# Kernel optimization log

Hardware: AMD Instinct MI355X
Metric: run time of the kernel (lower is better)

The kernel has to match this reference:

```python
import jax, jax.numpy as jnp
import numpy as np

V, S, D, H, L = 32000, 2048, 768, 12, 6
HD = D // H
EPS = 1e-5


def _sinusoidal_pe(s, d):
    pos = np.arange(s)[:, None].astype(np.float32)
    div = np.exp(np.arange(0, d, 2).astype(np.float32) * (-np.log(10000.0) / d))
    pe = np.zeros((s, d), dtype=np.float32)
    pe[:, 0::2] = np.sin(pos * div)
    pe[:, 1::2] = np.cos(pos * div)
    return jnp.asarray(pe)


def setup_inputs() -> dict:
    key = jax.random.key(0)
    ks = jax.random.split(key, 16)
    std = 0.02
    tok_emb = jax.random.normal(ks[0], (V, D), jnp.float32) * std
    tok_emb = tok_emb.at[1].set(0.0)  # padding_idx=1
    pos_enc = _sinusoidal_pe(S, D)
    attn_w = jax.random.normal(ks[1], (L, 3 * D, D), jnp.float32) * std
    attn_b = jnp.zeros((L, 3 * D), jnp.float32)
    proj_std = 0.02 / np.sqrt(2 * 6)
    proj_w = jax.random.normal(ks[2], (L, D, D), jnp.float32) * proj_std
    proj_b = jnp.zeros((L, D), jnp.float32)
    ln1_g = jnp.ones((L, D), jnp.float32); ln1_b = jnp.zeros((L, D), jnp.float32)
    ln2_g = jnp.ones((L, D), jnp.float32); ln2_b = jnp.zeros((L, D), jnp.float32)
    fc1_w = jax.random.normal(ks[3], (L, 4 * D, D), jnp.float32) * std
    fc1_b = jnp.zeros((L, 4 * D), jnp.float32)
    fc2_w = jax.random.normal(ks[4], (L, D, 4 * D), jnp.float32) * std
    fc2_b = jnp.zeros((L, D), jnp.float32)
    dec_w = jax.random.normal(ks[5], (V, D), jnp.float32) * std
    idx = jax.random.randint(ks[6], (2, S), 0, V)
    return dict(idx=idx, tok_emb=tok_emb, pos_enc=pos_enc, attn_w=attn_w,
                attn_b=attn_b, proj_w=proj_w, proj_b=proj_b, ln1_g=ln1_g,
                ln1_b=ln1_b, ln2_g=ln2_g, ln2_b=ln2_b, fc1_w=fc1_w,
                fc1_b=fc1_b, fc2_w=fc2_w, fc2_b=fc2_b, dec_w=dec_w)


def _ln(x, g, b):
    mu = jnp.mean(x, -1, keepdims=True)
    var = jnp.mean(jnp.square(x - mu), -1, keepdims=True)
    return (x - mu) * jax.lax.rsqrt(var + EPS) * g + b


def _forward(idx, tok_emb, pos_enc, attn_w, attn_b, proj_w, proj_b,
             ln1_g, ln1_b, ln2_g, ln2_b, fc1_w, fc1_b, fc2_w, fc2_b, dec_w):
    b, s = idx.shape
    x = tok_emb[idx] + pos_enc[:s]  # [b,s,d]
    for l in range(L):
        h = _ln(x, ln1_g[l], ln1_b[l])
        qkv = h @ attn_w[l].T + attn_b[l]
        q, k, v = jnp.split(qkv, 3, axis=-1)
        q = q.reshape(b, s, H, HD).transpose(0, 2, 1, 3)
        k = k.reshape(b, s, H, HD).transpose(0, 2, 1, 3)
        v = v.reshape(b, s, H, HD).transpose(0, 2, 1, 3)
        att = jnp.einsum('bhqd,bhkd->bhqk', q, k) * (1.0 / np.sqrt(HD))
        att = jax.nn.softmax(att, axis=-1)  # no causal mask in source
        y = jnp.einsum('bhqk,bhkd->bhqd', att, v)
        y = y.transpose(0, 2, 1, 3).reshape(b, s, D)
        x = x + (y @ proj_w[l].T + proj_b[l])
        h = _ln(x, ln2_g[l], ln2_b[l])
        h = jax.nn.gelu(h @ fc1_w[l].T + fc1_b[l])
        x = x + (h @ fc2_w[l].T + fc2_b[l])
    return x @ dec_w.T  # [b,s,V]


def reference(idx, tok_emb, pos_enc, attn_w, attn_b, proj_w, proj_b,
              ln1_g, ln1_b, ln2_g, ln2_b, fc1_w, fc1_b, fc2_w, fc2_b, dec_w):
    return _forward(idx, tok_emb, pos_enc, attn_w, attn_b, proj_w, proj_b,
                    ln1_g, ln1_b, ln2_g, ln2_b, fc1_w, fc1_b, fc2_w, fc2_b, dec_w)
```

## Files before the change

kernel.cpp:

```cpp
#include <hip/hip_runtime.h>
#include <hip/hip_bf16.h>
#include <stdint.h>


typedef unsigned short u16;
typedef __attribute__((ext_vector_type(8))) __bf16 bf16x8;
typedef __attribute__((ext_vector_type(4))) float f32x4;
typedef __attribute__((ext_vector_type(4))) unsigned int u32x4;
typedef __attribute__((ext_vector_type(4))) unsigned short u16x4;
typedef __attribute__((ext_vector_type(8))) unsigned short u16x8;

#define MFMA16(a, b, c) __builtin_amdgcn_mfma_f32_16x16x32_bf16((a), (b), (c), 0, 0, 0)

__device__ __forceinline__ float b2f(u16 u) {
  union { unsigned int i; float f; } x; x.i = ((unsigned int)u) << 16; return x.f;
}
__device__ __forceinline__ u16 f2b(float f) {
  union { float f; unsigned int i; } x; x.f = f;
  unsigned int r = x.i + 0x7fffu + ((x.i >> 16) & 1u);
  return (u16)(r >> 16);
}
__device__ __forceinline__ float gelu_f(float v) {
  const float t = 0.7978845608028654f * (v + 0.044715f * v * v * v);
  const float e = __expf(-2.f * fabsf(t));
  float th = (1.f - e) / (1.f + e);
  th = (t < 0.f) ? -th : th;
  return 0.5f * v * (1.f + th);
}
__device__ __forceinline__ void lds16(u16* l, const u16* g) {
  __builtin_amdgcn_global_load_lds(
      (const __attribute__((address_space(1))) unsigned int*)g,
      (__attribute__((address_space(3))) unsigned int*)l, 16, 0, 0);
}

__global__ __launch_bounds__(256) void conv_bf16_kernel(
    const float* __restrict__ src, u16* __restrict__ dst, int n8) {
  int i = blockIdx.x * 256 + threadIdx.x;
  const int stride = gridDim.x * 256;
  for (; i < n8; i += stride) {
    const f32x4 a = *(const f32x4*)&src[(size_t)i * 8];
    const f32x4 b = *(const f32x4*)&src[(size_t)i * 8 + 4];
    u16x8 p;
#pragma unroll
    for (int j = 0; j < 4; ++j) { p[j] = f2b(a[j]); p[4 + j] = f2b(b[j]); }
    *(u16x8*)&dst[(size_t)i * 8] = p;
  }
}

__global__ __launch_bounds__(256) void embed_kernel(
    const int* __restrict__ idx, const float* __restrict__ tok,
    const float* __restrict__ pos, float* __restrict__ x) {
  const int t = blockIdx.x;
  const int s = t & 2047;
  const int tid = threadIdx.x;
  const size_t to = (size_t)idx[t] * 768;
  const size_t po = (size_t)s * 768;
  float* xr = x + (size_t)t * 768;
#pragma unroll
  for (int i = 0; i < 3; ++i) {
    const int d = tid + i * 256;
    xr[d] = tok[to + d] + pos[po + d];
  }
}

__global__ __launch_bounds__(256) void ln_kernel(
    const float* __restrict__ x, const float* __restrict__ g,
    const float* __restrict__ b, u16* __restrict__ out) {
  const int w = threadIdx.x >> 6, lane = threadIdx.x & 63;
  const int row = blockIdx.x * 4 + w;
  const float* xr = x + (size_t)row * 768;
  f32x4 v[3];
#pragma unroll
  for (int i = 0; i < 3; ++i) v[i] = *(const f32x4*)&xr[i * 256 + lane * 4];
  float s = 0.f;
#pragma unroll
  for (int i = 0; i < 3; ++i)
#pragma unroll
    for (int j = 0; j < 4; ++j) s += v[i][j];
#pragma unroll
  for (int m = 1; m < 64; m <<= 1) s += __shfl_xor(s, m);
  const float mu = s * (1.f / 768.f);
  float q = 0.f;
#pragma unroll
  for (int i = 0; i < 3; ++i)
#pragma unroll
    for (int j = 0; j < 4; ++j) {
      const float d = v[i][j] - mu;
      q += d * d;
    }
#pragma unroll
  for (int m = 1; m < 64; m <<= 1) q += __shfl_xor(q, m);
  const float rs = rsqrtf(q * (1.f / 768.f) + 1e-5f);
  u16* orow = out + (size_t)row * 768;
#pragma unroll
  for (int i = 0; i < 3; ++i) {
    const f32x4 gg = *(const f32x4*)&g[i * 256 + lane * 4];
    const f32x4 bb = *(const f32x4*)&b[i * 256 + lane * 4];
    u16x4 o;
#pragma unroll
    for (int j = 0; j < 4; ++j) o[j] = f2b((v[i][j] - mu) * rs * gg[j] + bb[j]);
    *(u16x4*)&orow[i * 256 + lane * 4] = o;
  }
}

template <int MODE, int MFAST>
__global__ __launch_bounds__(256) void gemm_bb(
    const u16* __restrict__ A, const u16* __restrict__ B,
    const float* __restrict__ bias, u16* __restrict__ outb,
    float* __restrict__ outf, float* __restrict__ resid,
    u16* __restrict__ mirror, int N, int K) {
  __shared__ alignas(16) u16 As[2][128 * 64];
  __shared__ alignas(16) u16 Bs[2][128 * 64];
  const int tid = threadIdx.x;
  const int lane = tid & 63;
  const int w = tid >> 6;
  const int wr = (w >> 1) * 64;
  const int wc = (w & 1) * 64;
  const int fr = lane & 15;
  const int fg = lane >> 4;
  const int bn0 = (MFAST ? blockIdx.y : blockIdx.x) * 128;
  const int bm0 = (MFAST ? blockIdx.x : blockIdx.y) * 128;
  const int srow = tid >> 3;

  f32x4 acc[4][4] = {};

  auto stage = [&](int buf, int bk0) {
#pragma unroll
    for (int i = 0; i < 4; ++i) {
      const int row = i * 32 + srow;
      const int slot = (tid & 7) ^ (row & 7);
      lds16(&As[buf][(i * 256 + w * 64) * 8],
            &A[(size_t)(bm0 + row) * K + bk0 + slot * 8]);
      lds16(&Bs[buf][(i * 256 + w * 64) * 8],
            &B[(size_t)(bn0 + row) * K + bk0 + slot * 8]);
    }
  };

  stage(0, 0);
  int cur = 0;
  for (int bk0 = 0; bk0 < K; bk0 += 64) {
    __syncthreads();
    if (bk0 + 64 < K) stage(cur ^ 1, bk0 + 64);
#pragma unroll
    for (int kk = 0; kk < 64; kk += 32) {
      bf16x8 af[4], bfv[4];
#pragma unroll
      for (int m = 0; m < 4; ++m) {
        const int row = wr + m * 16 + fr;
        const int slot = ((kk >> 3) + fg) ^ (row & 7);
        af[m] = *(const bf16x8*)&As[cur][row * 64 + slot * 8];
      }
#pragma unroll
      for (int n = 0; n < 4; ++n) {
        const int row = wc + n * 16 + fr;
        const int slot = ((kk >> 3) + fg) ^ (row & 7);
        bfv[n] = *(const bf16x8*)&Bs[cur][row * 64 + slot * 8];
      }
#pragma unroll
      for (int m = 0; m < 4; ++m)
#pragma unroll
        for (int n = 0; n < 4; ++n)
          acc[m][n] = MFMA16(af[m], bfv[n], acc[m][n]);
    }
    cur ^= 1;
  }

#pragma unroll
  for (int n = 0; n < 4; ++n) {
    const int col = bn0 + wc + n * 16 + fr;
    const float bv = bias ? bias[col] : 0.0f;
#pragma unroll
    for (int m = 0; m < 4; ++m) {
#pragma unroll
      for (int r = 0; r < 4; ++r) {
        const int row = bm0 + wr + m * 16 + fg * 4 + r;
        float v = acc[m][n][r] + bv;
        if (MODE == 1) v = gelu_f(v);
        const size_t off = (size_t)row * N + col;
        if (MODE == 2) {
          const float nv = resid[off] + v;
          resid[off] = nv;
          if (mirror) mirror[off] = f2b(nv);
        } else if (MODE == 3) {
          __builtin_nontemporal_store(v, &outf[off]);
        } else {
          outb[off] = f2b(v);
        }
      }
    }
  }
}

template <int MODE>
__global__ __launch_bounds__(256) void gemm_bt(
    const u16* __restrict__ A, const float* __restrict__ B,
    const float* __restrict__ bias, u16* __restrict__ outb,
    float* __restrict__ outf, float* __restrict__ resid,
    u16* __restrict__ mirror, int N, int K) {
  __shared__ alignas(16) u16 As[128 * 64];
  __shared__ alignas(16) u16 Bs[128 * 64];
  const int tid = threadIdx.x;
  const int lane = tid & 63;
  const int w = tid >> 6;
  const int wr = (w >> 1) * 64;
  const int wc = (w & 1) * 64;
  const int fr = lane & 15;
  const int fg = lane >> 4;
  const int bn0 = blockIdx.x * 128;
  const int bm0 = blockIdx.y * 128;

  f32x4 acc[4][4] = {};

  for (int bk0 = 0; bk0 < K; bk0 += 64) {
    __syncthreads();
#pragma unroll
    for (int i = 0; i < 4; ++i) {
      const int c = i * 256 + tid;
      const int row = c >> 3;
      const int e0 = (c & 7) * 8;
      *(u32x4*)&As[row * 64 + e0] =
          *(const u32x4*)&A[(size_t)(bm0 + row) * K + bk0 + e0];
    }
#pragma unroll
    for (int i = 0; i < 8; ++i) {
      const int c = i * 256 + tid;
      const int row = c >> 4;
      const int e0 = (c & 15) * 4;
      const f32x4 fv = *(const f32x4*)&B[(size_t)(bn0 + row) * K + bk0 + e0];
      u16x4 pv;
#pragma unroll
      for (int j = 0; j < 4; ++j) pv[j] = f2b(fv[j]);
      *(u16x4*)&Bs[row * 64 + e0] = pv;
    }
    __syncthreads();
#pragma unroll
    for (int kk = 0; kk < 64; kk += 32) {
      bf16x8 af[4], bfv[4];
#pragma unroll
      for (int m = 0; m < 4; ++m)
        af[m] = *(const bf16x8*)&As[(wr + m * 16 + fr) * 64 + kk + fg * 8];
#pragma unroll
      for (int n = 0; n < 4; ++n)
        bfv[n] = *(const bf16x8*)&Bs[(wc + n * 16 + fr) * 64 + kk + fg * 8];
#pragma unroll
      for (int m = 0; m < 4; ++m)
#pragma unroll
        for (int n = 0; n < 4; ++n)
          acc[m][n] = MFMA16(af[m], bfv[n], acc[m][n]);
    }
  }

#pragma unroll
  for (int n = 0; n < 4; ++n) {
    const int col = bn0 + wc + n * 16 + fr;
    const float bv = bias ? bias[col] : 0.0f;
#pragma unroll
    for (int m = 0; m < 4; ++m) {
#pragma unroll
      for (int r = 0; r < 4; ++r) {
        const int row = bm0 + wr + m * 16 + fg * 4 + r;
        float v = acc[m][n][r] + bv;
        if (MODE == 1) v = gelu_f(v);
        const size_t off = (size_t)row * N + col;
        if (MODE == 2) {
          const float nv = resid[off] + v;
          resid[off] = nv;
          if (mirror) mirror[off] = f2b(nv);
        } else if (MODE == 3) {
          __builtin_nontemporal_store(v, &outf[off]);
        } else {
          outb[off] = f2b(v);
        }
      }
    }
  }
}

__global__ __launch_bounds__(256) void vtrans_kernel(
    const u16* __restrict__ qkv, u16* __restrict__ vt) {
  __shared__ u16 tile[64][72];
  const int tid = threadIdx.x;
  const int s0 = blockIdx.x * 64;
  const int hh = blockIdx.y;
  const int bb = blockIdx.z;
  const size_t tb = (size_t)bb * 2048 * 2304;
#pragma unroll
  for (int i = 0; i < 2; ++i) {
    const int c = i * 256 + tid;
    const int sl = c >> 3;
    const int d0 = (c & 7) * 8;
    *(u16x8*)&tile[sl][d0] =
        *(const u16x8*)&qkv[tb + (size_t)(s0 + sl) * 2304 + 1536 + hh * 64 + d0];
  }
  __syncthreads();
  const size_t vtb = (size_t)((bb * 12 + hh) * 64) * 2048;
#pragma unroll
  for (int i = 0; i < 2; ++i) {
    const int c = i * 256 + tid;
    const int d = c >> 3;
    const int so = (c & 7) * 8;
    u16x8 p;
#pragma unroll
    for (int j = 0; j < 8; ++j) p[j] = tile[so + j][d];
    *(u16x8*)&vt[vtb + (size_t)d * 2048 + s0 + so] = p;
  }
}

__global__ __launch_bounds__(256) void attn_kernel(
    const u16* __restrict__ qkv, const u16* __restrict__ vt,
    u16* __restrict__ y) {
  __shared__ alignas(16) u16 Ks[2][64 * 64];
  __shared__ alignas(16) u16 VTs[2][64 * 64];
  __shared__ alignas(16) u16 Ps[4][16 * 64];
  const int tid = threadIdx.x;
  const int lane = tid & 63;
  const int w = tid >> 6;
  const int fr = lane & 15;
  const int fg = lane >> 4;
  const int hh = blockIdx.y;
  const int bb = blockIdx.z;
  const size_t tb = (size_t)bb * 2048 * 2304;
  const size_t vtb = (size_t)((bb * 12 + hh) * 64) * 2048;
  const int q0 = blockIdx.x * 64 + w * 16;

  const bf16x8 qf0 =
      *(const bf16x8*)&qkv[tb + (size_t)(q0 + fr) * 2304 + hh * 64 + fg * 8];
  const bf16x8 qf1 =
      *(const bf16x8*)&qkv[tb + (size_t)(q0 + fr) * 2304 + hh * 64 + 32 + fg * 8];

  f32x4 oacc[4] = {};
  float mrow[4] = {-INFINITY, -INFINITY, -INFINITY, -INFINITY};
  float lrow[4] = {0.f, 0.f, 0.f, 0.f};

  const int chunkrow = lane >> 3;
  const int chunkslot = lane & 7;

  auto stage = [&](int buf, int kt) {
#pragma unroll
    for (int i = 0; i < 2; ++i) {
      const int row = (i * 4 + w) * 8 + chunkrow;
      const int slot = chunkslot ^ (row & 7);
      lds16(&Ks[buf][(i * 4 + w) * 512],
            &qkv[tb + (size_t)(kt + row) * 2304 + 768 + hh * 64 + slot * 8]);
      lds16(&VTs[buf][(i * 4 + w) * 512],
            &vt[vtb + (size_t)row * 2048 + kt + slot * 8]);
    }
  };

  stage(0, 0);
  int cur = 0;
  for (int kt = 0; kt < 2048; kt += 64) {
    __syncthreads();
    if (kt + 64 < 2048) stage(cur ^ 1, kt + 64);

    f32x4 s[4] = {};
#pragma unroll
    for (int kb = 0; kb < 4; ++kb) {
      const int row = kb * 16 + fr;
      const int sl0 = (fg) ^ (row & 7);
      const int sl1 = (4 + fg) ^ (row & 7);
      const bf16x8 k0 = *(const bf16x8*)&Ks[cur][row * 64 + sl0 * 8];
      const bf16x8 k1 = *(const bf16x8*)&Ks[cur][row * 64 + sl1 * 8];
      s[kb] = MFMA16(qf0, k0, s[kb]);
      s[kb] = MFMA16(qf1, k1, s[kb]);
    }

    float alpha[4];
    bool anyresc = false;
#pragma unroll
    for (int r = 0; r < 4; ++r) {
      float v[4];
#pragma unroll
      for (int kb = 0; kb < 4; ++kb) v[kb] = s[kb][r] * 0.125f;
      float mx = fmaxf(fmaxf(v[0], v[1]), fmaxf(v[2], v[3]));
      float mn = mrow[r];
      if (__all(mx <= mn)) {
        alpha[r] = 1.f;
      } else {
        mx = fmaxf(mx, __shfl_xor(mx, 1));
        mx = fmaxf(mx, __shfl_xor(mx, 2));
        mx = fmaxf(mx, __shfl_xor(mx, 4));
        mx = fmaxf(mx, __shfl_xor(mx, 8));
        mn = fmaxf(mrow[r], mx);
        alpha[r] = __expf(mrow[r] - mn);
        mrow[r] = mn;
        anyresc = true;
      }
      float p[4];
#pragma unroll
      for (int kb = 0; kb < 4; ++kb) p[kb] = __expf(v[kb] - mn);
      float ps = (p[0] + p[1]) + (p[2] + p[3]);
      ps += __shfl_xor(ps, 1);
      ps += __shfl_xor(ps, 2);
      ps += __shfl_xor(ps, 4);
      ps += __shfl_xor(ps, 8);
      lrow[r] = lrow[r] * alpha[r] + ps;
      const int q = fg * 4 + r;
#pragma unroll
      for (int kb = 0; kb < 4; ++kb) {
        const int kg = kb * 2 + (fr >> 3);
        Ps[w][q * 64 + ((kg ^ (q & 7)) << 3) + (fr & 7)] = f2b(p[kb]);
      }
    }
    if (anyresc) {
#pragma unroll
      for (int db = 0; db < 4; ++db)
#pragma unroll
        for (int r = 0; r < 4; ++r) oacc[db][r] *= alpha[r];
    }

#pragma unroll
    for (int kh = 0; kh < 2; ++kh) {
      const bf16x8 pa =
          *(const bf16x8*)&Ps[w][fr * 64 + (((kh * 4 + fg) ^ (fr & 7)) << 3)];
#pragma unroll
      for (int db = 0; db < 4; ++db) {
        const int row = db * 16 + fr;
        const int slot = (kh * 4 + fg) ^ (row & 7);
        const bf16x8 vb = *(const bf16x8*)&VTs[cur][row * 64 + slot * 8];
        oacc[db] = MFMA16(pa, vb, oacc[db]);
      }
    }
    cur ^= 1;
  }

#pragma unroll
  for (int db = 0; db < 4; ++db) {
#pragma unroll
    for (int r = 0; r < 4; ++r) {
      const int row = q0 + fg * 4 + r;
      y[(size_t)(bb * 2048 + row) * 768 + hh * 64 + db * 16 + fr] =
          f2b(oacc[db][r] / lrow[r]);
    }
  }
}

extern "C" void kernel_launch(void* const* d_in, const int* in_sizes, int n_in,
                              void* d_out, int out_size, void* d_ws,
                              size_t ws_size, hipStream_t stream) {
  const int*   idx   = (const int*)d_in[0];
  const float* tok   = (const float*)d_in[1];
  const float* pos   = (const float*)d_in[2];
  const float* attnw = (const float*)d_in[3];
  const float* attnb = (const float*)d_in[4];
  const float* projw = (const float*)d_in[5];
  const float* projb = (const float*)d_in[6];
  const float* ln1g  = (const float*)d_in[7];
  const float* ln1b  = (const float*)d_in[8];
  const float* ln2g  = (const float*)d_in[9];
  const float* ln2b  = (const float*)d_in[10];
  const float* fc1w  = (const float*)d_in[11];
  const float* fc1b  = (const float*)d_in[12];
  const float* fc2w  = (const float*)d_in[13];
  const float* fc2b  = (const float*)d_in[14];
  const float* decw  = (const float*)d_in[15];

  char* ws = (char*)d_ws;
  float* x = (float*)(ws);
  u16* h   = (u16*)(ws + 12582912);
  u16* qkv = (u16*)(ws + 18874368);
  u16* y   = (u16*)(ws + 37748736);
  u16* h2  = (u16*)(ws + 18874368);
  u16* vt  = h;

  const size_t WB0 = 44040192;
  u16* attnw_b = (u16*)(ws + WB0);
  u16* projw_b = (u16*)(ws + WB0 + 21233664);
  u16* fc1w_b  = (u16*)(ws + WB0 + 28311552);
  u16* fc2w_b  = (u16*)(ws + WB0 + 56623104);
  u16* decw_b  = (u16*)(ws + WB0 + 84934656);
  const size_t NEED = WB0 + 84934656 + 49152000;

  embed_kernel<<<4096, 256, 0, stream>>>(idx, tok, pos, x);

  if (ws_size >= NEED) {
    conv_bf16_kernel<<<2048, 256, 0, stream>>>(attnw, attnw_b, 10616832 / 8);
    conv_bf16_kernel<<<2048, 256, 0, stream>>>(projw, projw_b, 3538944 / 8);
    conv_bf16_kernel<<<2048, 256, 0, stream>>>(fc1w, fc1w_b, 14155776 / 8);
    conv_bf16_kernel<<<2048, 256, 0, stream>>>(fc2w, fc2w_b, 14155776 / 8);
    conv_bf16_kernel<<<2048, 256, 0, stream>>>(decw, decw_b, 24576000 / 8);

    for (int l = 0; l < 6; ++l) {
      ln_kernel<<<1024, 256, 0, stream>>>(x, ln1g + l * 768, ln1b + l * 768, h);
      gemm_bb<0, 0><<<dim3(18, 32), 256, 0, stream>>>(
          h, attnw_b + (size_t)l * 2304 * 768, attnb + l * 2304, qkv, nullptr,
          nullptr, nullptr, 2304, 768);
      vtrans_kernel<<<dim3(32, 12, 2), 256, 0, stream>>>(qkv, vt);
      attn_kernel<<<dim3(32, 12, 2), 256, 0, stream>>>(qkv, vt, y);
      gemm_bb<2, 0><<<dim3(6, 32), 256, 0, stream>>>(
          y, projw_b + (size_t)l * 768 * 768, projb + l * 768, nullptr, nullptr,
          x, nullptr, 768, 768);
      ln_kernel<<<1024, 256, 0, stream>>>(x, ln2g + l * 768, ln2b + l * 768, h);
      gemm_bb<1, 0><<<dim3(24, 32), 256, 0, stream>>>(
          h, fc1w_b + (size_t)l * 3072 * 768, fc1b + l * 3072, h2, nullptr,
          nullptr, nullptr, 3072, 768);
      gemm_bb<2, 0><<<dim3(6, 32), 256, 0, stream>>>(
          h2, fc2w_b + (size_t)l * 768 * 3072, fc2b + l * 768, nullptr, nullptr,
          x, (l == 5) ? h : nullptr, 768, 3072);
    }
    gemm_bb<3, 1><<<dim3(32, 250), 256, 0, stream>>>(
        h, decw_b, nullptr, nullptr, (float*)d_out, nullptr, nullptr, 32000,
        768);
  } else {
    for (int l = 0; l < 6; ++l) {
      ln_kernel<<<1024, 256, 0, stream>>>(x, ln1g + l * 768, ln1b + l * 768, h);
      gemm_bt<0><<<dim3(18, 32), 256, 0, stream>>>(
          h, attnw + (size_t)l * 2304 * 768, attnb + l * 2304, qkv, nullptr,
          nullptr, nullptr, 2304, 768);
      vtrans_kernel<<<dim3(32, 12, 2), 256, 0, stream>>>(qkv, vt);
      attn_kernel<<<dim3(32, 12, 2), 256, 0, stream>>>(qkv, vt, y);
      gemm_bt<2><<<dim3(6, 32), 256, 0, stream>>>(
          y, projw + (size_t)l * 768 * 768, projb + l * 768, nullptr, nullptr,
          x, nullptr, 768, 768);
      ln_kernel<<<1024, 256, 0, stream>>>(x, ln2g + l * 768, ln2b + l * 768, h);
      gemm_bt<1><<<dim3(24, 32), 256, 0, stream>>>(
          h, fc1w + (size_t)l * 3072 * 768, fc1b + l * 3072, h2, nullptr,
          nullptr, nullptr, 3072, 768);
      gemm_bt<2><<<dim3(6, 32), 256, 0, stream>>>(
          h2, fc2w + (size_t)l * 768 * 3072, fc2b + l * 768, nullptr, nullptr,
          x, (l == 5) ? h : nullptr, 768, 3072);
    }
    gemm_bt<3><<<dim3(250, 32), 256, 0, stream>>>(
        h, decw, nullptr, nullptr, (float*)d_out, nullptr, nullptr, 32000, 768);
  }
}
```

Baseline: 2.014 ms.

## Add 256x256-tile 8-wave GEMM with swizzled LDS and interleaved loads

Introduces a new bf16 MFMA GEMM kernel with 256x256 output tiles, 512 threads and 128KB of dynamic LDS. It uses an XOR-swizzled LDS layout, double-buffered half-K staging interleaved with the MFMA phases, and s_setprio around the MFMA bursts. The kernel replaces the 128x128 GEMM for QKV, proj, fc1 and the decoder; fc2 keeps the old kernel. The aim is more data reuse per tile and more latency hiding. In exchange, the smaller GEMMs get far fewer blocks (proj only 48) than the 256 CUs, which risks underutilisation.

```diff
diff --git a/kernel.cpp b/kernel.cpp
--- a/kernel.cpp
+++ b/kernel.cpp
@@ -100,6 +100,112 @@
 #pragma unroll
     for (int j = 0; j < 4; ++j) o[j] = f2b((v[i][j] - mu) * rs * gg[j] + bb[j]);
     *(u16x4*)&orow[i * 256 + lane * 4] = o;
+  }
+}
+
+#define G8PHASE(H, MH, LOADB)                                                 \
+  {                                                                           \
+    if (LOADB) {                                                              \
+      _Pragma("unroll") for (int n = 0; n < 4; ++n) {                         \
+        const int row = wn * 64 + n * 16 + fr;                                \
+        bfv[n] = *(const bf16x8*)&Bs_[bufr * 16384 + (H) * 8192 + row * 32 +  \
+                                      ((fg ^ ((row ^ (row >> 2)) & 3)) << 3)];\
+      }                                                                       \
+    }                                                                         \
+    bf16x8 af[4];                                                             \
+    _Pragma("unroll") for (int m = 0; m < 4; ++m) {                           \
+      const int row = wm * 128 + (MH) * 64 + m * 16 + fr;                     \
+      af[m] = *(const bf16x8*)&As_[bufr * 16384 + (H) * 8192 + row * 32 +     \
+                                   ((fg ^ ((row ^ (row >> 2)) & 3)) << 3)];   \
+    }                                                                         \
+    __builtin_amdgcn_s_setprio(1);                                            \
+    _Pragma("unroll") for (int m = 0; m < 4; ++m)                             \
+      _Pragma("unroll") for (int n = 0; n < 4; ++n)                           \
+        acc[(MH) * 4 + m][n] = MFMA16(af[m], bfv[n], acc[(MH) * 4 + m][n]);   \
+    __builtin_amdgcn_s_setprio(0);                                            \
+  }
+
+template <int MODE, int MFAST>
+__global__ __launch_bounds__(512, 2) void gemm8(
+    const u16* __restrict__ A, const u16* __restrict__ B,
+    const float* __restrict__ bias, u16* __restrict__ outb,
+    float* __restrict__ outf, float* __restrict__ resid, int N, int K) {
+  extern __shared__ u16 sm8[];
+  u16* As_ = sm8;
+  u16* Bs_ = sm8 + 32768;
+  const int tid = threadIdx.x;
+  const int lane = tid & 63;
+  const int w = tid >> 6;
+  const int wm = w >> 2;
+  const int wn = w & 3;
+  const int fr = lane & 15;
+  const int fg = lane >> 4;
+  const int bn0 = (MFAST ? blockIdx.y : blockIdx.x) * 256;
+  const int bm0 = (MFAST ? blockIdx.x : blockIdx.y) * 256;
+  const int nt = K >> 6;
+
+  f32x4 acc[8][4] = {};
+  bf16x8 bfv[4];
+
+  auto stage = [&](u16* lbase, const u16* __restrict__ M, int rbase, int k0) {
+#pragma unroll
+    for (int i = 0; i < 2; ++i) {
+      const int c = i * 512 + tid;
+      const int row = c >> 2;
+      const int slot = (c & 3) ^ ((row ^ (row >> 2)) & 3);
+      lds16(lbase + (i * 512 + w * 64) * 8,
+            M + (size_t)(rbase + row) * K + k0 + slot * 8);
+    }
+  };
+
+  stage(As_ + 0, A, bm0, 0);
+  stage(Bs_ + 0, B, bn0, 0);
+  stage(As_ + 8192, A, bm0, 32);
+  stage(Bs_ + 8192, B, bn0, 32);
+
+  int bufr = 0;
+  for (int t = 0; t < nt; ++t) {
+    const int tn = (t + 1 < nt) ? t + 1 : t;
+    const int bufw = bufr ^ 1;
+    const int kn = tn * 64;
+    asm volatile("s_waitcnt vmcnt(4)" ::: "memory");
+    __builtin_amdgcn_sched_barrier(0);
+    __builtin_amdgcn_s_barrier();
+    stage(As_ + bufw * 16384, A, bm0, kn);
+    G8PHASE(0, 0, true)
+    stage(Bs_ + bufw * 16384, B, bn0, kn);
+    G8PHASE(0, 1, false)
+    asm volatile("s_waitcnt vmcnt(4)" ::: "memory");
+    __builtin_amdgcn_sched_barrier(0);
+    __builtin_amdgcn_s_barrier();
+    stage(As_ + bufw * 16384 + 8192, A, bm0, kn + 32);
+    G8PHASE(1, 0, true)
+    stage(Bs_ + bufw * 16384 + 8192, B, bn0, kn + 32);
+    G8PHASE(1, 1, false)
+    bufr ^= 1;
+  }
+
+#pragma unroll
+  for (int n = 0; n < 4; ++n) {
+    const int col = bn0 + wn * 64 + n * 16 + fr;
+    const float bv = bias ? bias[col] : 0.0f;
+#pragma unroll
+    for (int i = 0; i < 8; ++i) {
+#pragma unroll
+      for (int r = 0; r < 4; ++r) {
+        const int row = bm0 + wm * 128 + i * 16 + fg * 4 + r;
+        float v = acc[i][n][r] + bv;
+        if (MODE == 1) v = gelu_f(v);
+        const size_t off = (size_t)row * N + col;
+        if (MODE == 2) {
+          resid[off] += v;
+        } else if (MODE == 3) {
+          __builtin_nontemporal_store(v, &outf[off]);
+        } else {
+          outb[off] = f2b(v);
+        }
+      }
+    }
   }
 }
 
@@ -482,25 +588,24 @@
 
     for (int l = 0; l < 6; ++l) {
       ln_kernel<<<1024, 256, 0, stream>>>(x, ln1g + l * 768, ln1b + l * 768, h);
-      gemm_bb<0, 0><<<dim3(18, 32), 256, 0, stream>>>(
+      gemm8<0, 0><<<dim3(9, 16), 512, 131072, stream>>>(
           h, attnw_b + (size_t)l * 2304 * 768, attnb + l * 2304, qkv, nullptr,
-          nullptr, nullptr, 2304, 768);
+          nullptr, 2304, 768);
       vtrans_kernel<<<dim3(32, 12, 2), 256, 0, stream>>>(qkv, vt);
       attn_kernel<<<dim3(32, 12, 2), 256, 0, stream>>>(qkv, vt, y);
-      gemm_bb<2, 0><<<dim3(6, 32), 256, 0, stream>>>(
+      gemm8<2, 0><<<dim3(3, 16), 512, 131072, stream>>>(
           y, projw_b + (size_t)l * 768 * 768, projb + l * 768, nullptr, nullptr,
-          x, nullptr, 768, 768);
+          x, 768, 768);
       ln_kernel<<<1024, 256, 0, stream>>>(x, ln2g + l * 768, ln2b + l * 768, h);
-      gemm_bb<1, 0><<<dim3(24, 32), 256, 0, stream>>>(
+      gemm8<1, 0><<<dim3(12, 16), 512, 131072, stream>>>(
           h, fc1w_b + (size_t)l * 3072 * 768, fc1b + l * 3072, h2, nullptr,
-          nullptr, nullptr, 3072, 768);
+          nullptr, 3072, 768);
       gemm_bb<2, 0><<<dim3(6, 32), 256, 0, stream>>>(
           h2, fc2w_b + (size_t)l * 768 * 3072, fc2b + l * 768, nullptr, nullptr,
           x, (l == 5) ? h : nullptr, 768, 3072);
     }
-    gemm_bb<3, 1><<<dim3(32, 250), 256, 0, stream>>>(
-        h, decw_b, nullptr, nullptr, (float*)d_out, nullptr, nullptr, 32000,
-        768);
+    gemm8<3, 1><<<dim3(16, 125), 512, 131072, stream>>>(
+        h, decw_b, nullptr, nullptr, (float*)d_out, nullptr, 32000, 768);
   } else {
     for (int l = 0; l < 6; ++l) {
       ln_kernel<<<1024, 256, 0, stream>>>(x, ln1g + l * 768, ln1b + l * 768, h);
```

Measured after the change: 2.006 ms. No clear change (-0.4%).
